# Optimization experiments

Hardware: AMD Instinct MI355X
Metric: run time of the kernel (lower is better)

Reference implementation:

```python
import jax, jax.numpy as jnp
import numpy as np

N_NODES = 100000
N_EDGES = 1600000
N_GRAPHS = 128
IN_DIM, HID, OUT_DIM, DOC_DIM = 64, 128, 32, 768
LAYERS = 3


def setup_inputs() -> dict:
    key = jax.random.key(0)
    ks = jax.random.split(key, 24)
    s = 0.05
    inp = {
        "x": jax.random.normal(ks[0], (N_NODES, IN_DIM), jnp.float32),
        "doc_features": jax.random.normal(ks[1], (N_GRAPHS, DOC_DIM), jnp.float32),
        "edge_index": jax.random.randint(ks[2], (2, N_EDGES), 0, N_NODES, jnp.int64),
        "batch": jnp.sort(jax.random.randint(ks[3], (N_NODES,), 0, N_GRAPHS, jnp.int64)),
        # parameters (stored as [in, out] so y = x @ W + b)
        "node_w": jax.random.normal(ks[4], (IN_DIM, HID), jnp.float32) * s,
        "node_b": jnp.zeros((HID,), jnp.float32),
        "ggnn_w": jax.random.normal(ks[5], (LAYERS, HID, HID), jnp.float32) * s,
        "gru_w_ih": jax.random.normal(ks[6], (HID, 3 * HID), jnp.float32) * s,
        "gru_b_ih": jnp.zeros((3 * HID,), jnp.float32),
        "gru_w_hh": jax.random.normal(ks[7], (HID, 3 * HID), jnp.float32) * s,
        "gru_b_hh": jnp.zeros((3 * HID,), jnp.float32),
        "doc_w": jax.random.normal(ks[8], (DOC_DIM, HID), jnp.float32) * s,
        "doc_b": jnp.zeros((HID,), jnp.float32),
        "ln_g": jnp.ones((2 * HID,), jnp.float32),
        "ln_b": jnp.zeros((2 * HID,), jnp.float32),
        "fus_w": jax.random.normal(ks[9], (2 * HID, HID), jnp.float32) * s,
        "fus_b": jnp.zeros((HID,), jnp.float32),
        "task_w": jax.random.normal(ks[10], (HID, OUT_DIM), jnp.float32) * s,
        "task_b": jnp.zeros((OUT_DIM,), jnp.float32),
        "time_w": jax.random.normal(ks[11], (HID, 1), jnp.float32) * s,
        "time_b": jnp.zeros((1,), jnp.float32),
    }
    return inp


def _gru(m, h, w_ih, b_ih, w_hh, b_hh):
    gi = m @ w_ih + b_ih  # [N, 3H]
    gh = h @ w_hh + b_hh
    ir, iz, in_ = jnp.split(gi, 3, axis=-1)
    hr, hz, hn = jnp.split(gh, 3, axis=-1)
    r = jax.nn.sigmoid(ir + hr)
    z = jax.nn.sigmoid(iz + hz)
    n = jnp.tanh(in_ + r * hn)
    return (1.0 - z) * n + z * h


def reference(x, doc_features, node_w, node_b, ggnn_w, gru_w_ih, gru_b_ih,
              gru_w_hh, gru_b_hh, doc_w, doc_b, ln_g, ln_b, fus_w, fus_b,
              task_w, task_b, time_w, time_b, edge_index, batch):
    N = x.shape[0]
    src, dst = edge_index[0], edge_index[1]
    # node projection + ReLU
    h = jax.nn.relu(x @ node_w + node_b)  # [N, H]
    # GatedGraphConv: 3 layers of (linear -> scatter-add over edges -> GRU)
    for i in range(LAYERS):
        m = h @ ggnn_w[i]                              # [N, H]
        agg = jax.ops.segment_sum(m[src], dst, num_segments=N)  # scatter-add
        h = _gru(agg, h, gru_w_ih, gru_b_ih, gru_w_hh, gru_b_hh)
    # global mean pool over graphs
    sums = jax.ops.segment_sum(h, batch, num_segments=N_GRAPHS)  # [G, H]
    cnt = jax.ops.segment_sum(jnp.ones((N,), h.dtype), batch, num_segments=N_GRAPHS)
    pooled = sums / jnp.maximum(cnt, 1.0)[:, None]
    # doc projection + fusion head
    doc_emb = jax.nn.relu(doc_features @ doc_w + doc_b)  # [G, H]
    fusion = jnp.concatenate([pooled, doc_emb], axis=1)  # [G, 2H]
    mu = jnp.mean(fusion, axis=-1, keepdims=True)
    var = jnp.mean(jnp.square(fusion - mu), axis=-1, keepdims=True)
    fusion = (fusion - mu) * jax.lax.rsqrt(var + 1e-5) * ln_g + ln_b
    fusion = jax.nn.relu(fusion @ fus_w + fus_b)  # dropout is identity (eval)
    task_output = fusion @ task_w + task_b
    time_output = fusion @ time_w + time_b
    return (task_output, time_output)
```

## Files before the change

kernel.cpp:

```cpp
#include <hip/hip_runtime.h>

#define N_NODES  100000
#define N_EDGES  1600000
#define N_GRAPHS 128

#define BSH      8
#define BNODES   (1 << BSH)
#define NBUCK    391
#define NBLK_P1  512
#define EPB      (N_EDGES / NBLK_P1)
#define BKT_SCAN_N   (NBUCK * NBLK_P1)
#define SCAN_BLK_BKT 196
#define SCAN_BLK_NODE 98

typedef unsigned short u16;
typedef unsigned int   u32;
typedef __attribute__((ext_vector_type(8))) short short8;
typedef __attribute__((ext_vector_type(4))) float f32x4;

__device__ __forceinline__ float bf2f(u16 v) {
  union { u32 i; float f; } u; u.i = ((u32)v) << 16; return u.f;
}
__device__ __forceinline__ u16 f2bf(float f) {
  union { float f; u32 i; } u; u.f = f;
  u32 r = (u.i + 0x7fffu + ((u.i >> 16) & 1u)) >> 16;
  return (u16)r;
}
__device__ __forceinline__ float sigmoid_f(float x) { return 1.f / (1.f + __expf(-x)); }
__device__ __forceinline__ float tanh_f(float x) {
  x = fminf(15.f, fmaxf(-15.f, x));
  float e = __expf(2.f * x);
  return (e - 1.f) / (e + 1.f);
}
__device__ __forceinline__ int geti(const int* __restrict__ p, int i, int is64) {
  return p[is64 ? (2 * i) : i];
}

__global__ void detect_i64_kernel(const int* __restrict__ ei, const int* __restrict__ batch,
                                  int* __restrict__ flags) {
  int lane = threadIdx.x;
  {
    long long q = (long long)lane * (3200000 / 2 - 1) / 63;
    int pos = (int)(2 * q + 1);
    unsigned long long m = __ballot(ei[pos] != 0);
    if (lane == 0) flags[0] = (m == 0ull) ? 1 : 0;
  }
  {
    long long q = (long long)lane * (100000 / 2 - 1) / 63;
    int pos = (int)(2 * q + 1);
    unsigned long long m = __ballot(batch[pos] != 0);
    if (lane == 0) flags[1] = (m == 0ull) ? 1 : 0;
  }
}


__global__ __launch_bounds__(256)
void bucket_hist(const int* __restrict__ ei, const int* __restrict__ flags,
                 int* __restrict__ bcounts) {
  __shared__ int h[NBUCK];
  const int f = flags[0];
  for (int b = threadIdx.x; b < NBUCK; b += 256) h[b] = 0;
  __syncthreads();
  const int e0 = blockIdx.x * EPB;
  for (int i = threadIdx.x; i < EPB; i += 256) {
    int d = geti(ei, N_EDGES + e0 + i, f);
    atomicAdd(&h[d >> BSH], 1);
  }
  __syncthreads();
  for (int b = threadIdx.x; b < NBUCK; b += 256)
    bcounts[b * NBLK_P1 + blockIdx.x] = h[b];
}

__global__ __launch_bounds__(256)
void bucket_scatter(const int* __restrict__ ei, const int* __restrict__ flags,
                    const int* __restrict__ bbases, u32* __restrict__ bedges) {
  __shared__ int cur[NBUCK];
  const int f = flags[0];
  for (int b = threadIdx.x; b < NBUCK; b += 256)
    cur[b] = bbases[b * NBLK_P1 + blockIdx.x];
  __syncthreads();
  const int e0 = blockIdx.x * EPB;
  for (int i = threadIdx.x; i < EPB; i += 256) {
    int e = e0 + i;
    int d = geti(ei, N_EDGES + e, f);
    int s = geti(ei, e, f);
    int pos = atomicAdd(&cur[d >> BSH], 1);
    bedges[pos] = ((u32)(d & (BNODES - 1)) << 17) | (u32)s;
  }
}

__global__ __launch_bounds__(256)
void node_count(const u32* __restrict__ bedges, const int* __restrict__ bbases,
                int* __restrict__ counts) {
  __shared__ int h[BNODES];
  const int b = blockIdx.x;
  for (int i = threadIdx.x; i < BNODES; i += 256) h[i] = 0;
  __syncthreads();
  const int beg = bbases[b * NBLK_P1];
  const int end = (b + 1 < NBUCK) ? bbases[(b + 1) * NBLK_P1] : N_EDGES;
  for (int e = beg + threadIdx.x; e < end; e += 256)
    atomicAdd(&h[bedges[e] >> 17], 1);
  __syncthreads();
  const int node0 = b << BSH;
  for (int i = threadIdx.x; i < BNODES; i += 256)
    if (node0 + i < N_NODES) counts[node0 + i] = h[i];
}

__global__ __launch_bounds__(256)
void final_scatter(const u32* __restrict__ bedges, const int* __restrict__ bbases,
                   const int* __restrict__ offs, int* __restrict__ ssrc) {
  __shared__ int cur[BNODES];
  const int b = blockIdx.x;
  const int node0 = b << BSH;
  for (int i = threadIdx.x; i < BNODES; i += 256)
    cur[i] = (node0 + i < N_NODES) ? offs[node0 + i] : 0;
  __syncthreads();
  const int beg = bbases[b * NBLK_P1];
  const int end = (b + 1 < NBUCK) ? bbases[(b + 1) * NBLK_P1] : N_EDGES;
  for (int e = beg + threadIdx.x; e < end; e += 256) {
    u32 v = bedges[e];
    int pos = atomicAdd(&cur[v >> 17], 1);
    ssrc[pos] = (int)(v & 0x1FFFFu);
  }
}

__global__ __launch_bounds__(1024)
void scanA_kernel(const int* __restrict__ counts, int n, int* __restrict__ blocksums) {
  __shared__ int red[16];
  int i = blockIdx.x * 1024 + threadIdx.x;
  int v = (i < n) ? counts[i] : 0;
  for (int o = 32; o > 0; o >>= 1) v += __shfl_down(v, o, 64);
  int wv = threadIdx.x >> 6, lane = threadIdx.x & 63;
  if (lane == 0) red[wv] = v;
  __syncthreads();
  if (threadIdx.x < 16) {
    int s = red[threadIdx.x];
    for (int o = 8; o > 0; o >>= 1) s += __shfl_down(s, o, 64);
    if (threadIdx.x == 0) blocksums[blockIdx.x] = s;
  }
}

__global__ void scanB_kernel(const int* __restrict__ blocksums, int nblocks,
                             int* __restrict__ blockbase, int* __restrict__ total_out) {
  if (threadIdx.x == 0) {
    int run = 0;
    for (int b = 0; b < nblocks; ++b) { blockbase[b] = run; run += blocksums[b]; }
    if (total_out) *total_out = run;
  }
}

__global__ __launch_bounds__(1024)
void scanC_kernel(const int* __restrict__ counts, int n, const int* __restrict__ blockbase,
                  int* __restrict__ offsets) {
  __shared__ int buf[1024];
  int t = threadIdx.x;
  int i = blockIdx.x * 1024 + t;
  int v = (i < n) ? counts[i] : 0;
  buf[t] = v;
  __syncthreads();
  for (int o = 1; o < 1024; o <<= 1) {
    int add = (t >= o) ? buf[t - o] : 0;
    __syncthreads();
    buf[t] += add;
    __syncthreads();
  }
  if (i < n) offsets[i] = buf[t] - v + blockbase[blockIdx.x];
}

__global__ void transpose_kernel(const float* __restrict__ in, u16* __restrict__ out, int K, int N) {
  int i = blockIdx.x * 256 + threadIdx.x;
  if (i < K * N) {
    int k = i / N, n = i % N;
    out[n * K + k] = f2bf(in[i]);
  }
}

__global__ void wprime_kernel(const float* __restrict__ ggnn_w, const float* __restrict__ w_ih,
                              float* __restrict__ wp) {
  int i = blockIdx.x * 256 + threadIdx.x;
  if (i >= 3 * 128 * 384) return;
  int l = i / (128 * 384), r = i % (128 * 384), k = r / 384, c = r % 384;
  const float* W = ggnn_w + l * 128 * 128;
  float s = 0.f;
  for (int j = 0; j < 128; ++j) s += W[k * 128 + j] * w_ih[j * 384 + c];
  wp[i] = s;
}

__global__ void build_b2q_kernel(const float* __restrict__ wp, const float* __restrict__ w_hh,
                                 u16* __restrict__ b2q) {
  int g = blockIdx.x * 256 + threadIdx.x;
  if (g >= 98304) return;
  int r = g;
  int e    = r & 7;   r >>= 3;
  int col  = r & 127; r >>= 7;
  int quad = r & 3;   r >>= 2;
  int gate = r % 3;   r /= 3;
  int ci   = r;
  int k = ci * 32 + quad * 8 + e;
  int n_lin = gate * 128 + col;
  float v = (k < 128) ? wp[k * 384 + n_lin] : w_hh[(k - 128) * 384 + n_lin];
  b2q[g] = f2bf(v);
}

__global__ __launch_bounds__(256)
void nodeproj_gemm(const float* __restrict__ A, const u16* __restrict__ BT,
                   const float* __restrict__ bias, u16* __restrict__ out, int M)
{
  constexpr int K_DIM = 64, N_DIM = 128, NT = 8, NCHUNK = 2;
  __shared__ u16 B_lds[N_DIM * 40];
  const int tid = threadIdx.x, lane = tid & 63, w = tid >> 6;
  const int strip = blockIdx.x * 64;
  const int ksub = (lane >> 4) * 8;
  union Frag { uint4 u; short8 s; };
  Frag af[NCHUNK];
  const int m_node = strip + w * 16 + (lane & 15);
  const bool avalid = (m_node < M);
#pragma unroll
  for (int ci = 0; ci < NCHUNK; ++ci) {
    int k0 = ci * 32 + ksub;
    short8 sv = {0,0,0,0,0,0,0,0};
    if (avalid) {
      const float* p = A + (size_t)m_node * K_DIM + k0;
      float4 f0 = *(const float4*)p;
      float4 f1 = *(const float4*)(p + 4);
      sv[0]=(short)f2bf(f0.x); sv[1]=(short)f2bf(f0.y); sv[2]=(short)f2bf(f0.z); sv[3]=(short)f2bf(f0.w);
      sv[4]=(short)f2bf(f1.x); sv[5]=(short)f2bf(f1.y); sv[6]=(short)f2bf(f1.z); sv[7]=(short)f2bf(f1.w);
    }
    af[ci].s = sv;
  }
  f32x4 acc[NT];
#pragma unroll
  for (int t = 0; t < NT; ++t) acc[t] = {0.f, 0.f, 0.f, 0.f};
  const int boff = (lane & 15) * 40 + ksub;
#pragma unroll
  for (int ci = 0; ci < NCHUNK; ++ci) {
    if (ci) __syncthreads();
    for (int g = tid; g < N_DIM * 4; g += 256) {
      int n = g >> 2, ko = g & 3;
      uint4 bv = *(const uint4*)(BT + (size_t)n * K_DIM + ci * 32 + ko * 8);
      *(uint4*)(&B_lds[n * 40 + ko * 8]) = bv;
    }
    __syncthreads();
    short8 a = af[ci].s;
#pragma unroll
    for (int t = 0; t < NT; ++t) {
      const short8 b = *(const short8*)(&B_lds[t * 16 * 40 + boff]);
      acc[t] = __builtin_amdgcn_mfma_f32_16x16x32_bf16(a, b, acc[t], 0, 0, 0);
    }
  }
  const int mrow = (lane >> 4) * 4;
#pragma unroll
  for (int t = 0; t < NT; ++t) {
    int col = t * 16 + (lane & 15);
    float bv = bias[col];
#pragma unroll
    for (int r = 0; r < 4; ++r) {
      int node = strip + w * 16 + mrow + r;
      if (node < M) out[(size_t)node * N_DIM + col] = f2bf(fmaxf(acc[t][r] + bv, 0.f));
    }
  }
}

__global__ __launch_bounds__(512, 6)
void gru_gemm(const u16* __restrict__ agg, const u16* __restrict__ h,
              const u16* __restrict__ b2q, const float* __restrict__ b_ih,
              const float* __restrict__ b_hh, u16* __restrict__ hout, int M)
{
  __shared__ u16 Blds[24576];
  const int tid  = threadIdx.x;
  const int lane = tid & 63;
  const int w    = tid >> 6;
  const int bid  = blockIdx.x;
  const int xcd = bid & 7, idx = bid >> 3;
  const int linear = ((xcd < 6) ? xcd * 391 : 6 * 391 + (xcd - 6) * 390) + idx;
  const int ch2  = linear & 1;
  const int strip = (linear >> 1) * 64;
  const int rw   = (w & 3) * 16;
  const int cb   = (w >> 2) * 32;
  const int lrow = lane & 15;
  const int quad = lane >> 4;

  const int node = strip + rw + lrow;
  const bool nv = (node < M);

  union Frag { uint4 u; short8 s8; };
  Frag a[2];
  const uint4 zz = {0u, 0u, 0u, 0u};
  auto lda = [&](int ci, int p) {
    const u16* ap = (ci < 4) ? (agg + ci * 32 + quad * 8) : (h + (ci - 4) * 32 + quad * 8);
    a[p].u = nv ? *(const uint4*)(ap + (size_t)node * 128) : zz;
  };

  auto stageB = [&](int half) {
#pragma unroll
    for (int k = 0; k < 6; ++k) {
      const int i4  = tid + k * 512;
      const int run = i4 >> 6, off = i4 & 63;
      const int ci  = run / 12, rem = run - ci * 12;
      const int gt  = rem >> 2, qd = rem & 3;
      const size_t so = (size_t)(half * 4 + ci) * 12288 + gt * 4096 + qd * 1024
                        + ch2 * 512 + off * 8;
      *(uint4*)(&Blds[run * 512 + off * 8]) = *(const uint4*)(b2q + so);
    }
  };

  lda(0, 0);
  lda(1, 1);
  stageB(0);

  f32x4 ar[2], az[2], ain[2], ahn[2];
#pragma unroll
  for (int t = 0; t < 2; ++t) {
    ar[t] = {0.f,0.f,0.f,0.f}; az[t] = {0.f,0.f,0.f,0.f};
    ain[t] = {0.f,0.f,0.f,0.f}; ahn[t] = {0.f,0.f,0.f,0.f};
  }

  __syncthreads();

#pragma unroll
  for (int ci = 0; ci < 8; ++ci) {
    if (ci == 4) {
      __syncthreads();
      stageB(1);
      __syncthreads();
    }
    const int p = ci & 1;
    short8 A = a[p].s8;
    if (ci < 6) lda(ci + 2, p);
#pragma unroll
    for (int t = 0; t < 2; ++t) {
      const u16* lb = &Blds[(ci & 3) * 6144 + quad * 512 + (cb + t * 16 + lrow) * 8];
      short8 br = *(const short8*)(lb);
      short8 bz = *(const short8*)(lb + 2048);
      short8 bg = *(const short8*)(lb + 4096);
      ar[t] = __builtin_amdgcn_mfma_f32_16x16x32_bf16(A, br, ar[t], 0, 0, 0);
      az[t] = __builtin_amdgcn_mfma_f32_16x16x32_bf16(A, bz, az[t], 0, 0, 0);
      if (ci < 4) ain[t] = __builtin_amdgcn_mfma_f32_16x16x32_bf16(A, bg, ain[t], 0, 0, 0);
      else        ahn[t] = __builtin_amdgcn_mfma_f32_16x16x32_bf16(A, bg, ahn[t], 0, 0, 0);
    }
  }

  __syncthreads();
  u16* Olds = (u16*)Blds;
#pragma unroll
  for (int t = 0; t < 2; ++t) {
    const int cl = cb + t * 16 + lrow;
    const int c  = ch2 * 64 + cl;
    const float brr = b_ih[c] + b_hh[c];
    const float bzz = b_ih[128 + c] + b_hh[128 + c];
    const float bin = b_ih[256 + c];
    const float bhn = b_hh[256 + c];
#pragma unroll
    for (int r = 0; r < 4; ++r) {
      const int lr   = rw + quad * 4 + r;
      const int nrow = strip + lr;
      u16 val = 0;
      if (nrow < M) {
        float rg = sigmoid_f(ar[t][r] + brr);
        float zg = sigmoid_f(az[t][r] + bzz);
        float hv = ahn[t][r] + bhn;
        float ng = tanh_f(ain[t][r] + bin + rg * hv);
        float hp = bf2f(h[(size_t)nrow * 128 + c]);
        val = f2bf((1.f - zg) * ng + zg * hp);
      }
      Olds[lr * 64 + cl] = val;
    }
  }
  __syncthreads();
  {
    const int row = tid >> 3, c8 = tid & 7;
    const int nrow = strip + row;
    if (nrow < M)
      *(uint4*)(&hout[(size_t)nrow * 128 + ch2 * 64 + c8 * 8]) =
          *(const uint4*)(&Olds[row * 64 + c8 * 8]);
  }
}

__global__ __launch_bounds__(256)
void agg_kernel(const u16* __restrict__ m, const int* __restrict__ ssrc,
                const int* __restrict__ offsets, u16* __restrict__ agg)
{
  int node = blockIdx.x * 4 + (threadIdx.x >> 6);
  int lane = threadIdx.x & 63;
  if (node >= N_NODES) return;
  const int g = lane >> 4, l = lane & 15;
  int beg = offsets[node], end = offsets[node + 1];
  float s[8] = {0.f,0.f,0.f,0.f,0.f,0.f,0.f,0.f};
  for (int e = beg; e < end; e += 16) {
    uint4 v0 = {0u,0u,0u,0u}, v1 = {0u,0u,0u,0u};
    uint4 v2 = {0u,0u,0u,0u}, v3 = {0u,0u,0u,0u};
    int e0 = e + g, e1 = e + 4 + g, e2 = e + 8 + g, e3 = e + 12 + g;
    if (e0 < end) { int src = ssrc[e0]; v0 = *(const uint4*)(m + (size_t)src * 128 + l * 8); }
    if (e1 < end) { int src = ssrc[e1]; v1 = *(const uint4*)(m + (size_t)src * 128 + l * 8); }
    if (e2 < end) { int src = ssrc[e2]; v2 = *(const uint4*)(m + (size_t)src * 128 + l * 8); }
    if (e3 < end) { int src = ssrc[e3]; v3 = *(const uint4*)(m + (size_t)src * 128 + l * 8); }
    u32 w0[4] = {v0.x, v0.y, v0.z, v0.w};
    u32 w1[4] = {v1.x, v1.y, v1.z, v1.w};
    u32 w2[4] = {v2.x, v2.y, v2.z, v2.w};
    u32 w3[4] = {v3.x, v3.y, v3.z, v3.w};
#pragma unroll
    for (int i = 0; i < 4; ++i) {
      s[2*i]   += (bf2f((u16)(w0[i] & 0xffffu)) + bf2f((u16)(w1[i] & 0xffffu)))
                + (bf2f((u16)(w2[i] & 0xffffu)) + bf2f((u16)(w3[i] & 0xffffu)));
      s[2*i+1] += (bf2f((u16)(w0[i] >> 16))     + bf2f((u16)(w1[i] >> 16)))
                + (bf2f((u16)(w2[i] >> 16))     + bf2f((u16)(w3[i] >> 16)));
    }
  }
#pragma unroll
  for (int i = 0; i < 8; ++i) {
    s[i] += __shfl_xor(s[i], 16, 64);
    s[i] += __shfl_xor(s[i], 32, 64);
  }
  if (g == 0) {
    uint4 o;
    o.x = (u32)f2bf(s[0]) | ((u32)f2bf(s[1]) << 16);
    o.y = (u32)f2bf(s[2]) | ((u32)f2bf(s[3]) << 16);
    o.z = (u32)f2bf(s[4]) | ((u32)f2bf(s[5]) << 16);
    o.w = (u32)f2bf(s[6]) | ((u32)f2bf(s[7]) << 16);
    *(uint4*)(agg + (size_t)node * 128 + l * 8) = o;
  }
}

__global__ __launch_bounds__(256)
void pool_kernel(const u16* __restrict__ h, const int* __restrict__ batch,
                 const int* __restrict__ flags, float* __restrict__ sums)
{
  const int c = threadIdx.x & 127;
  const int half = threadIdx.x >> 7;
  const int base = blockIdx.x * 128;
  const int f = flags[1];
  int gcur = -1; float s = 0.f;
  for (int i = half; i < 128; i += 2) {
    int n = base + i;
    if (n >= N_NODES) break;
    int g = geti(batch, n, f);
    if (g != gcur) {
      if (gcur >= 0) atomicAdd(&sums[gcur * 128 + c], s);
      s = 0.f; gcur = g;
    }
    s += bf2f(h[(size_t)n * 128 + c]);
  }
  if (gcur >= 0) atomicAdd(&sums[gcur * 128 + c], s);
}

__global__ __launch_bounds__(256)
void head2_kernel(const float* __restrict__ sums, const int* __restrict__ batch,
                  const int* __restrict__ flags,
                  const float* __restrict__ doc, const float* __restrict__ doc_w, const float* __restrict__ doc_b,
                  const float* __restrict__ ln_g, const float* __restrict__ ln_b,
                  const float* __restrict__ fus_w, const float* __restrict__ fus_b,
                  const float* __restrict__ task_w, const float* __restrict__ task_b,
                  const float* __restrict__ time_w, const float* __restrict__ time_b,
                  float* __restrict__ out_task, float* __restrict__ out_time)
{
  const int g = blockIdx.x;
  const int t = threadIdx.x;
  __shared__ float fusion[256];
  __shared__ float fh[128];
  __shared__ float dpart[256];
  __shared__ int seg[2];

  if (t < 2) {
    int f = flags[1];
    int target = g + t, lo = 0, hi = N_NODES;
    while (lo < hi) { int mid = (lo + hi) >> 1; if (geti(batch, mid, f) < target) lo = mid + 1; else hi = mid; }
    seg[t] = lo;
  }
  {
    int c = t & 127, kh = t >> 7;
    float s = 0.f;
    for (int k = kh * 384; k < kh * 384 + 384; ++k) s += doc[g * 768 + k] * doc_w[k * 128 + c];
    dpart[t] = s;
  }
  __syncthreads();

  if (t < 128) {
    float cnt = (float)(seg[1] - seg[0]);
    fusion[t] = sums[g * 128 + t] / fmaxf(cnt, 1.f);
  } else {
    int c = t - 128;
    fusion[t] = fmaxf(dpart[c] + dpart[c + 128] + doc_b[c], 0.f);
  }
  __syncthreads();

  float mu = 0.f;
  for (int i = 0; i < 256; ++i) mu += fusion[i];
  mu *= (1.f / 256.f);
  float var = 0.f;
  for (int i = 0; i < 256; ++i) { float d = fusion[i] - mu; var += d * d; }
  var *= (1.f / 256.f);
  float inv = rsqrtf(var + 1e-5f);
  float norm = (fusion[t] - mu) * inv * ln_g[t] + ln_b[t];
  __syncthreads();
  fusion[t] = norm;
  __syncthreads();

  if (t < 128) {
    float s = 0.f;
    for (int k = 0; k < 256; ++k) s += fusion[k] * fus_w[k * 128 + t];
    s += fus_b[t];
    fh[t] = fmaxf(s, 0.f);
  }
  __syncthreads();

  if (t < 32) {
    float s = 0.f;
    for (int k = 0; k < 128; ++k) s += fh[k] * task_w[k * 32 + t];
    s += task_b[t];
    out_task[g * 32 + t] = s;
  }
  if (t == 32) {
    float s = 0.f;
    for (int k = 0; k < 128; ++k) s += fh[k] * time_w[k];
    s += time_b[0];
    out_time[g] = s;
  }
}

extern "C" void kernel_launch(void* const* d_in, const int* in_sizes, int n_in,
                              void* d_out, int out_size, void* d_ws, size_t ws_size,
                              hipStream_t stream)
{
  const float* x        = (const float*)d_in[0];
  const float* doc      = (const float*)d_in[1];
  const int*   ei       = (const int*)d_in[2];
  const int*   batch    = (const int*)d_in[3];
  const float* node_w   = (const float*)d_in[4];
  const float* node_b   = (const float*)d_in[5];
  const float* ggnn_w   = (const float*)d_in[6];
  const float* gru_w_ih = (const float*)d_in[7];
  const float* gru_b_ih = (const float*)d_in[8];
  const float* gru_w_hh = (const float*)d_in[9];
  const float* gru_b_hh = (const float*)d_in[10];
  const float* doc_w    = (const float*)d_in[11];
  const float* doc_b    = (const float*)d_in[12];
  const float* ln_g     = (const float*)d_in[13];
  const float* ln_b     = (const float*)d_in[14];
  const float* fus_w    = (const float*)d_in[15];
  const float* fus_b    = (const float*)d_in[16];
  const float* task_w   = (const float*)d_in[17];
  const float* task_b   = (const float*)d_in[18];
  const float* time_w   = (const float*)d_in[19];
  const float* time_b   = (const float*)d_in[20];

  char* ws = (char*)d_ws;
  size_t off = 0;
  auto alloc = [&](size_t bytes) -> void* {
    void* p = ws + off;
    off = (off + bytes + 255) & ~(size_t)255;
    return p;
  };
  u16* aggb    = (u16*)alloc((size_t)N_NODES * 128 * 2);
  u16* hA      = (u16*)alloc((size_t)N_NODES * 128 * 2);
  u16* hB      = (u16*)alloc((size_t)N_NODES * 128 * 2);
  u16* nwT     = (u16*)alloc(64 * 128 * 2);
  u16* b2q     = (u16*)alloc(3 * 98304 * 2);
  float* wp    = (float*)alloc(3 * 128 * 384 * 4);
  float* sums  = (float*)alloc(N_GRAPHS * 128 * 4);
  int* counts  = (int*)alloc((size_t)N_NODES * 4);
  int* offs    = (int*)alloc((size_t)(N_NODES + 1) * 4);
  int* ssrc    = (int*)alloc((size_t)N_EDGES * 4);
  int* bsum    = (int*)alloc(SCAN_BLK_BKT * 4);
  int* bbase   = (int*)alloc(SCAN_BLK_BKT * 4);
  int* flags   = (int*)alloc(2 * 4);

  u32* bedges  = (u32*)aggb;
  int* bcounts = (int*)((char*)aggb + 6400000);
  int* bbases  = (int*)((char*)aggb + 7200768);

  hipMemsetAsync(sums, 0, (size_t)N_GRAPHS * 128 * 4, stream);

  detect_i64_kernel<<<1, 64, 0, stream>>>(ei, batch, flags);

  bucket_hist<<<NBLK_P1, 256, 0, stream>>>(ei, flags, bcounts);
  scanA_kernel<<<SCAN_BLK_BKT, 1024, 0, stream>>>(bcounts, BKT_SCAN_N, bsum);
  scanB_kernel<<<1, 64, 0, stream>>>(bsum, SCAN_BLK_BKT, bbase, (int*)nullptr);
  scanC_kernel<<<SCAN_BLK_BKT, 1024, 0, stream>>>(bcounts, BKT_SCAN_N, bbase, bbases);
  bucket_scatter<<<NBLK_P1, 256, 0, stream>>>(ei, flags, bbases, bedges);
  node_count<<<NBUCK, 256, 0, stream>>>(bedges, bbases, counts);
  scanA_kernel<<<SCAN_BLK_NODE, 1024, 0, stream>>>(counts, N_NODES, bsum);
  scanB_kernel<<<1, 64, 0, stream>>>(bsum, SCAN_BLK_NODE, bbase, offs + N_NODES);
  scanC_kernel<<<SCAN_BLK_NODE, 1024, 0, stream>>>(counts, N_NODES, bbase, offs);
  final_scatter<<<NBUCK, 256, 0, stream>>>(bedges, bbases, offs, ssrc);

  transpose_kernel<<<(64 * 128 + 255) / 256, 256, 0, stream>>>(node_w, nwT, 64, 128);
  wprime_kernel<<<(3 * 128 * 384 + 255) / 256, 256, 0, stream>>>(ggnn_w, gru_w_ih, wp);
  for (int l = 0; l < 3; ++l)
    build_b2q_kernel<<<(98304 + 255) / 256, 256, 0, stream>>>(
        wp + l * 128 * 384, gru_w_hh, b2q + (size_t)l * 98304);

  const int GB = (N_NODES + 63) / 64;
  const int GBGRU = ((N_NODES + 63) / 64) * 2;
  nodeproj_gemm<<<GB, 256, 0, stream>>>(x, nwT, node_b, hA, N_NODES);

  u16* hcur = hA;
  u16* hnext = hB;
  for (int l = 0; l < 3; ++l) {
    agg_kernel<<<(N_NODES + 3) / 4, 256, 0, stream>>>(hcur, ssrc, offs, aggb);
    gru_gemm<<<GBGRU, 512, 0, stream>>>(aggb, hcur, b2q + (size_t)l * 98304,
                                        gru_b_ih, gru_b_hh, hnext, N_NODES);
    u16* tmp = hcur; hcur = hnext; hnext = tmp;
  }

  pool_kernel<<<(N_NODES + 127) / 128, 256, 0, stream>>>(hcur, batch, flags, sums);

  float* out_task = (float*)d_out;
  float* out_time = out_task + N_GRAPHS * 32;
  head2_kernel<<<N_GRAPHS, 256, 0, stream>>>(sums, batch, flags, doc, doc_w, doc_b, ln_g, ln_b,
                                             fus_w, fus_b, task_w, task_b, time_w, time_b,
                                             out_task, out_time);
}
```

Measured before the change: 627.4 us.

## Compute full 128-column GRU tile per block with double-buffered weight staging

Each gru_gemm block now covers all 128 output columns of a 64-row strip instead of half, so the A fragments (agg and h) are loaded once rather than twice across two blocks, and the grid is halved. Weight chunks are staged per K-slice into two alternating LDS buffers, with the next chunk prefetched while the current one feeds MFMAs and one barrier per iteration. Accumulator registers double, which may lower occupancy under the 512x6 launch bound, and the XCD remapping is retuned for the smaller grid.

```diff
diff --git a/kernel.cpp b/kernel.cpp
--- a/kernel.cpp
+++ b/kernel.cpp
@@ -266,17 +266,16 @@
               const u16* __restrict__ b2q, const float* __restrict__ b_ih,
               const float* __restrict__ b_hh, u16* __restrict__ hout, int M)
 {
-  __shared__ u16 Blds[24576];
+  __shared__ u16 Bbuf[2][12288];
   const int tid  = threadIdx.x;
   const int lane = tid & 63;
   const int w    = tid >> 6;
   const int bid  = blockIdx.x;
   const int xcd = bid & 7, idx = bid >> 3;
-  const int linear = ((xcd < 6) ? xcd * 391 : 6 * 391 + (xcd - 6) * 390) + idx;
-  const int ch2  = linear & 1;
-  const int strip = (linear >> 1) * 64;
+  const int linear = ((xcd < 3) ? xcd * 196 : 3 * 196 + (xcd - 3) * 195) + idx;
+  const int strip = linear * 64;
   const int rw   = (w & 3) * 16;
-  const int cb   = (w >> 2) * 32;
+  const int ch   = (w >> 2) * 64;
   const int lrow = lane & 15;
   const int quad = lane >> 4;
 
@@ -291,26 +290,22 @@
     a[p].u = nv ? *(const uint4*)(ap + (size_t)node * 128) : zz;
   };
 
-  auto stageB = [&](int half) {
-#pragma unroll
-    for (int k = 0; k < 6; ++k) {
-      const int i4  = tid + k * 512;
-      const int run = i4 >> 6, off = i4 & 63;
-      const int ci  = run / 12, rem = run - ci * 12;
-      const int gt  = rem >> 2, qd = rem & 3;
-      const size_t so = (size_t)(half * 4 + ci) * 12288 + gt * 4096 + qd * 1024
-                        + ch2 * 512 + off * 8;
-      *(uint4*)(&Blds[run * 512 + off * 8]) = *(const uint4*)(b2q + so);
+  auto stageB = [&](int ci, int buf) {
+    const u16* src = b2q + (size_t)ci * 12288;
+#pragma unroll
+    for (int k = 0; k < 3; ++k) {
+      int i4 = tid + k * 512;
+      *(uint4*)(&Bbuf[buf][i4 * 8]) = *(const uint4*)(src + i4 * 8);
     }
   };
 
   lda(0, 0);
   lda(1, 1);
-  stageB(0);
-
-  f32x4 ar[2], az[2], ain[2], ahn[2];
-#pragma unroll
-  for (int t = 0; t < 2; ++t) {
+  stageB(0, 0);
+
+  f32x4 ar[4], az[4], ain[4], ahn[4];
+#pragma unroll
+  for (int t = 0; t < 4; ++t) {
     ar[t] = {0.f,0.f,0.f,0.f}; az[t] = {0.f,0.f,0.f,0.f};
     ain[t] = {0.f,0.f,0.f,0.f}; ahn[t] = {0.f,0.f,0.f,0.f};
   }
@@ -319,33 +314,28 @@
 
 #pragma unroll
   for (int ci = 0; ci < 8; ++ci) {
-    if (ci == 4) {
-      __syncthreads();
-      stageB(1);
-      __syncthreads();
-    }
     const int p = ci & 1;
+    if (ci < 7) stageB(ci + 1, p ^ 1);
     short8 A = a[p].s8;
     if (ci < 6) lda(ci + 2, p);
 #pragma unroll
-    for (int t = 0; t < 2; ++t) {
-      const u16* lb = &Blds[(ci & 3) * 6144 + quad * 512 + (cb + t * 16 + lrow) * 8];
+    for (int t = 0; t < 4; ++t) {
+      const u16* lb = &Bbuf[p][quad * 1024 + (ch + t * 16 + lrow) * 8];
       short8 br = *(const short8*)(lb);
-      short8 bz = *(const short8*)(lb + 2048);
-      short8 bg = *(const short8*)(lb + 4096);
+      short8 bz = *(const short8*)(lb + 4096);
+      short8 bg = *(const short8*)(lb + 8192);
       ar[t] = __builtin_amdgcn_mfma_f32_16x16x32_bf16(A, br, ar[t], 0, 0, 0);
       az[t] = __builtin_amdgcn_mfma_f32_16x16x32_bf16(A, bz, az[t], 0, 0, 0);
       if (ci < 4) ain[t] = __builtin_amdgcn_mfma_f32_16x16x32_bf16(A, bg, ain[t], 0, 0, 0);
       else        ahn[t] = __builtin_amdgcn_mfma_f32_16x16x32_bf16(A, bg, ahn[t], 0, 0, 0);
     }
-  }
-
-  __syncthreads();
-  u16* Olds = (u16*)Blds;
-#pragma unroll
-  for (int t = 0; t < 2; ++t) {
-    const int cl = cb + t * 16 + lrow;
-    const int c  = ch2 * 64 + cl;
+    __syncthreads();
+  }
+
+  u16* Olds = (u16*)Bbuf;
+#pragma unroll
+  for (int t = 0; t < 4; ++t) {
+    const int c = ch + t * 16 + lrow;
     const float brr = b_ih[c] + b_hh[c];
     const float bzz = b_ih[128 + c] + b_hh[128 + c];
     const float bin = b_ih[256 + c];
@@ -363,16 +353,17 @@
         float hp = bf2f(h[(size_t)nrow * 128 + c]);
         val = f2bf((1.f - zg) * ng + zg * hp);
       }
-      Olds[lr * 64 + cl] = val;
-    }
-  }
-  __syncthreads();
-  {
-    const int row = tid >> 3, c8 = tid & 7;
+      Olds[lr * 128 + c] = val;
+    }
+  }
+  __syncthreads();
+#pragma unroll
+  for (int rr = 0; rr < 2; ++rr) {
+    const int row = (tid >> 4) + rr * 32;
+    const int c16 = tid & 15;
     const int nrow = strip + row;
     if (nrow < M)
-      *(uint4*)(&hout[(size_t)nrow * 128 + ch2 * 64 + c8 * 8]) =
-          *(const uint4*)(&Olds[row * 64 + c8 * 8]);
+      *(uint4*)(&hout[(size_t)nrow * 128 + c16 * 8]) = *(const uint4*)(&Olds[row * 128 + c16 * 8]);
   }
 }
 
@@ -590,15 +581,14 @@
         wp + l * 128 * 384, gru_w_hh, b2q + (size_t)l * 98304);
 
   const int GB = (N_NODES + 63) / 64;
-  const int GBGRU = ((N_NODES + 63) / 64) * 2;
   nodeproj_gemm<<<GB, 256, 0, stream>>>(x, nwT, node_b, hA, N_NODES);
 
   u16* hcur = hA;
   u16* hnext = hB;
   for (int l = 0; l < 3; ++l) {
     agg_kernel<<<(N_NODES + 3) / 4, 256, 0, stream>>>(hcur, ssrc, offs, aggb);
-    gru_gemm<<<GBGRU, 512, 0, stream>>>(aggb, hcur, b2q + (size_t)l * 98304,
-                                        gru_b_ih, gru_b_hh, hnext, N_NODES);
+    gru_gemm<<<GB, 512, 0, stream>>>(aggb, hcur, b2q + (size_t)l * 98304,
+                                     gru_b_ih, gru_b_hh, hnext, N_NODES);
     u16* tmp = hcur; hcur = hnext; hnext = tmp;
   }
 
```

Result: slower. 707.1 us (+12.7%).
